# Kernel tuning notes

Measured on AMD Instinct MI355X. Metric: run time of the kernel, lower is better.

Reference implementation:

```python
import jax, jax.numpy as jnp
import numpy as np
import math

B, L, N, DIM, H = 2, 8, 1024, 512, 8
DH = DIM // H

def setup_inputs() -> dict:
    key = jax.random.key(0)
    ks = jax.random.split(key, 9)
    s = 1.0 / math.sqrt(DIM)
    return {
        "x": jax.random.normal(ks[0], (B, L, N, DIM), dtype=jnp.float32),
        "Wq": jax.random.normal(ks[1], (DIM, DIM), dtype=jnp.float32) * s,
        "bq": jnp.zeros((DIM,), dtype=jnp.float32),
        "Wk": jax.random.normal(ks[2], (DIM, DIM), dtype=jnp.float32) * s,
        "bk": jnp.zeros((DIM,), dtype=jnp.float32),
        "Wv": jax.random.normal(ks[3], (DIM, DIM), dtype=jnp.float32) * s,
        "bv": jnp.zeros((DIM,), dtype=jnp.float32),
        "Wo": jax.random.normal(ks[4], (DIM, DIM), dtype=jnp.float32) * s,
        "bo": jnp.zeros((DIM,), dtype=jnp.float32),
    }

def _split_heads(t):
    # 'b l n (h d) -> b l h n d'
    b, l, n, _ = t.shape
    return t.reshape(b, l, n, H, DH).transpose(0, 1, 3, 2, 4)

def reference(x, Wq, bq, Wk, bk, Wv, bv, Wo, bo):
    q = _split_heads(x @ Wq.T + bq)
    # FAITHFUL BUG: source maps (q, v, k) -> (q_mat, k_mat, v_mat),
    # so the "keys" come from the v projection and "values" from the k projection.
    k_mat = _split_heads(x @ Wv.T + bv)
    v_mat = _split_heads(x @ Wk.T + bk)
    # scale is sqrt(Dh * num_heads) = sqrt(dim), as in the source
    scores = jnp.einsum('blhnd,blhmd->blhnm', q, k_mat) / math.sqrt(DIM)
    weights = jax.nn.softmax(scores, axis=-1)
    inter = jnp.einsum('blhnm,blhmd->blhnd', weights, v_mat)
    # 'b l h n d -> b l n (h d)'
    inter = inter.transpose(0, 1, 3, 2, 4).reshape(x.shape[0], x.shape[1], x.shape[2], DIM)
    return inter @ Wo.T + bo
```

## Files before the change

### kernel.cpp

```cpp
#include <hip/hip_runtime.h>
#include <stdint.h>

#define DIMC 512
#define NSEQ 1024
#define BLT  16
#define NHEAD 8
#define DHD  64
#define MTOT (BLT*NSEQ)

typedef float f32x4 __attribute__((ext_vector_type(4)));
typedef float f32x16 __attribute__((ext_vector_type(16)));
typedef short s16x8 __attribute__((ext_vector_type(8)));
typedef short s16x4 __attribute__((ext_vector_type(4)));

__device__ __forceinline__ unsigned short f2bf(float f) {
    unsigned int u = __float_as_uint(f);
    u += 0x7fffu + ((u >> 16) & 1u);
    return (unsigned short)(u >> 16);
}
__device__ __forceinline__ float bf2f(unsigned short h) {
    return __uint_as_float(((unsigned int)h) << 16);
}

#define QSCALE (0.04419417382415922f * 1.4426950408889634f)

__device__ __forceinline__ void gll16(const void* g, void* l) {
    __builtin_amdgcn_global_load_lds(
        (const __attribute__((address_space(1))) void*)g,
        (__attribute__((address_space(3))) void*)l, 16, 0, 0);
}

__device__ __forceinline__ unsigned int cvtpk(float lo, float hi) {
    unsigned int r;
    asm("v_cvt_pk_bf16_f32 %0, %1, %2" : "=v"(r) : "v"(lo), "v"(hi));
    return r;
}

__device__ __forceinline__ void pl32swap(unsigned int &a, unsigned int &b) {
    asm volatile("v_permlane32_swap_b32 %0, %1" : "+v"(a), "+v"(b));
}

__device__ __forceinline__ bool detect_bf16(const unsigned short* x) {
    int t = threadIdx.x & 63;
    unsigned short v = x[2 * t];
    int e = (v >> 7) & 0xFF;
    unsigned long long ball = __ballot(e < 100 || e > 137);
    return __popcll(ball) < 16;
}

struct ConvArgs {
    const void* src[9];
    unsigned short* dst[9];
};

__global__ __launch_bounds__(256) void conv_kernel(ConvArgs a,
                                                   const unsigned short* __restrict__ xdet) {
    const bool isbf = detect_bf16(xdet);
    int b = blockIdx.x;
    int seg, idx;
    if (b < 4096)      { seg = 0; idx = (b * 256 + threadIdx.x) * 8; }
    else if (b < 4608) { int t = b - 4096; seg = 1 + (t >> 7);
                         idx = (((t & 127) * 256) + threadIdx.x) * 8; }
    else               { int i = threadIdx.x * 8; seg = 5 + (i >> 9); idx = i & 511; }
    const void* s = a.src[seg];
    unsigned short* d = a.dst[seg];
    if (isbf) {
        *(uint4*)(d + idx) = *(const uint4*)((const unsigned short*)s + idx);
    } else {
        float4 t0 = *(const float4*)((const float*)s + idx);
        float4 t1 = *(const float4*)((const float*)s + idx + 4);
        ushort4 v0{f2bf(t0.x), f2bf(t0.y), f2bf(t0.z), f2bf(t0.w)};
        ushort4 v1{f2bf(t1.x), f2bf(t1.y), f2bf(t1.z), f2bf(t1.w)};
        *(ushort4*)(d + idx)     = v0;
        *(ushort4*)(d + idx + 4) = v1;
    }
}

__device__ __forceinline__ void gemm_core_async(
    const unsigned short* __restrict__ Ap, const unsigned short* __restrict__ Wp,
    int mBase, int nBase, unsigned short* Al, unsigned short* Bl, f32x4 acc[4][4])
{
    const int wave = threadIdx.x >> 6;
    const int lane = threadIdx.x & 63;
    const int lr = lane & 15, lg = lane >> 4;
    const int wm = wave >> 1, wn = wave & 1;
    const int srow = lane >> 3;
    const int scol = (lane & 7) * 8;

    #pragma unroll
    for (int a = 0; a < 4; ++a)
        #pragma unroll
        for (int b = 0; b < 4; ++b) acc[a][b] = (f32x4){0.f, 0.f, 0.f, 0.f};

    for (int k0 = 0; k0 < DIMC; k0 += 64) {
        #pragma unroll
        for (int i = 0; i < 4; ++i) {
            int rbase = (wave * 4 + i) * 8;
            gll16(Ap + (long)(mBase + rbase + srow) * DIMC + k0 + scol, Al + rbase * 64);
            gll16(Wp + (long)(nBase + rbase + srow) * DIMC + k0 + scol, Bl + rbase * 64);
        }
        __syncthreads();

        #pragma unroll
        for (int kk = 0; kk < 64; kk += 32) {
            s16x8 af[4], bf_[4];
            #pragma unroll
            for (int a = 0; a < 4; ++a)
                af[a] = *(const s16x8*)&Al[(wm * 64 + a * 16 + lr) * 64 + kk + lg * 8];
            #pragma unroll
            for (int b = 0; b < 4; ++b)
                bf_[b] = *(const s16x8*)&Bl[(wn * 64 + b * 16 + lr) * 64 + kk + lg * 8];
            #pragma unroll
            for (int a = 0; a < 4; ++a)
                #pragma unroll
                for (int b = 0; b < 4; ++b)
                    acc[a][b] = __builtin_amdgcn_mfma_f32_16x16x32_bf16(af[a], bf_[b], acc[a][b], 0, 0, 0);
        }
        __syncthreads();
    }
}

__global__ __launch_bounds__(256) void proj_kernel(
    const unsigned short* __restrict__ xb,
    const unsigned short* __restrict__ Wqb, const unsigned short* __restrict__ Wkb,
    const unsigned short* __restrict__ Wvb,
    const unsigned short* __restrict__ bqb, const unsigned short* __restrict__ bkb,
    const unsigned short* __restrict__ bvb,
    unsigned short* __restrict__ Q, unsigned short* __restrict__ K,
    unsigned short* __restrict__ Vt)
{
    const int z = blockIdx.z;
    const unsigned short* Wp = (z == 0) ? Wqb : ((z == 1) ? Wvb : Wkb);
    const unsigned short* bp = (z == 0) ? bqb : ((z == 1) ? bvb : bkb);
    unsigned short* outp = (z == 0) ? Q : ((z == 1) ? K : Vt);
    const float oscale = (z == 0) ? QSCALE : 1.0f;

    const int mBase = blockIdx.x * 128;
    const int nBase = blockIdx.y * 128;
    const int lane = threadIdx.x & 63;
    const int lr = lane & 15, lg = lane >> 4;
    const int wm = (threadIdx.x >> 6) >> 1, wn = (threadIdx.x >> 6) & 1;

    __shared__ unsigned short Al[128 * 64];
    __shared__ unsigned short Bl[128 * 64];
    f32x4 acc[4][4];
    gemm_core_async(xb, Wp, mBase, nBase, Al, Bl, acc);

    #pragma unroll
    for (int b = 0; b < 4; ++b) {
        int j = nBase + wn * 64 + b * 16 + lr;
        float bb = bf2f(bp[j]);
        int h = j >> 6, d = j & 63;
        #pragma unroll
        for (int a = 0; a < 4; ++a) {
            int m0 = mBase + wm * 64 + a * 16 + lg * 4;
            int bl = m0 >> 10, n0 = m0 & 1023;
            if (z == 2) {
                ushort4 pk;
                unsigned short* p = (unsigned short*)&pk;
                #pragma unroll
                for (int r = 0; r < 4; ++r) p[r] = f2bf(acc[a][b][r] + bb);
                *(ushort4*)&outp[(((bl << 3) + h) << 16) + (d << 10) + n0] = pk;
            } else {
                #pragma unroll
                for (int r = 0; r < 4; ++r) {
                    float v = (acc[a][b][r] + bb) * oscale;
                    outp[(((bl << 3) + h) << 16) + ((n0 + r) << 6) + d] = f2bf(v);
                }
            }
        }
    }
}

__global__ __launch_bounds__(256) void out_gemm_kernel(
    const unsigned short* __restrict__ inter, const unsigned short* __restrict__ Wob,
    const unsigned short* __restrict__ bob, void* __restrict__ outp,
    const unsigned short* __restrict__ xdet)
{
    const bool isbf = detect_bf16(xdet);
    const int mBase = blockIdx.x * 128;
    const int nBase = blockIdx.y * 128;
    const int lane = threadIdx.x & 63;
    const int lr = lane & 15, lg = lane >> 4;
    const int wm = (threadIdx.x >> 6) >> 1, wn = (threadIdx.x >> 6) & 1;

    __shared__ unsigned short Al[128 * 64];
    __shared__ unsigned short Bl[128 * 64];
    f32x4 acc[4][4];
    gemm_core_async(inter, Wob, mBase, nBase, Al, Bl, acc);

    #pragma unroll
    for (int b = 0; b < 4; ++b) {
        int j = nBase + wn * 64 + b * 16 + lr;
        float bb = bf2f(bob[j]);
        #pragma unroll
        for (int a = 0; a < 4; ++a) {
            #pragma unroll
            for (int r = 0; r < 4; ++r) {
                long m = mBase + wm * 64 + a * 16 + lg * 4 + r;
                float v = acc[a][b][r] + bb;
                if (isbf) ((unsigned short*)outp)[m * DIMC + j] = f2bf(v);
                else      ((float*)outp)[m * DIMC + j] = v;
            }
        }
    }
}

#define SWZ(row, col) ((row) * 64 + ((col) ^ (((row) & 7) * 8)))

__global__ __launch_bounds__(256, 3) void attn_kernel(
    const unsigned short* __restrict__ Q, const unsigned short* __restrict__ K,
    const unsigned short* __restrict__ Vt, unsigned short* __restrict__ inter)
{
    const int b = blockIdx.x;
    const int bh = b & 127;
    const int qt = b >> 7;
    const int tid = threadIdx.x;
    const int wave = tid >> 6;
    const int lane = tid & 63;
    const int l31 = lane & 31;
    const int hi = lane >> 5;

    const unsigned short* Qb = Q + (long)bh * (NSEQ * DHD);
    const int qbase = qt * 128 + wave * 32;

    s16x8 qf[4];
    #pragma unroll
    for (int k16 = 0; k16 < 4; ++k16)
        qf[k16] = *(const s16x8*)&Qb[(qbase + l31) * DHD + k16 * 16 + hi * 8];

    __shared__ unsigned short Kl[2][64 * 64];
    __shared__ unsigned short Vl[2][64 * 64];

    const int srow = tid >> 3;
    const int scol = ((tid & 7) * 8) ^ ((srow & 7) * 8);
    const unsigned short* kp = K  + (long)bh * (NSEQ * DHD) + srow * DHD  + scol;
    const unsigned short* vp = Vt + (long)bh * (NSEQ * DHD) + srow * NSEQ + scol;

    auto stage = [&](int buf, long ko, long vo) {
        unsigned short* Kb_ = &Kl[buf][0];
        unsigned short* Vb_ = &Vl[buf][0];
        gll16(kp + ko,         Kb_ + wave * 512);
        gll16(kp + ko + 2048,  Kb_ + wave * 512 + 2048);
        gll16(vp + vo,         Vb_ + wave * 512);
        gll16(vp + vo + 32768, Vb_ + wave * 512 + 2048);
    };

    f32x16 o[2];
    f32x16 lacc;
    f32x16 zero16;
    #pragma unroll
    for (int r = 0; r < 16; ++r) { o[0][r] = 0.f; o[1][r] = 0.f; lacc[r] = 0.f; zero16[r] = 0.f; }
    const s16x8 ones8 = {(short)0x3F80, (short)0x3F80, (short)0x3F80, (short)0x3F80,
                         (short)0x3F80, (short)0x3F80, (short)0x3F80, (short)0x3F80};

    stage(0, 0, 0);
    __syncthreads();

    #pragma unroll 2
    for (int kt = 0; kt < 16; ++kt) {
        const int cur = kt & 1;
        if (kt < 15)
            stage(cur ^ 1, (long)(kt + 1) * (64 * DHD), (long)(kt + 1) * 64);

        const unsigned short* Kc = &Kl[cur][0];
        const unsigned short* Vc = &Vl[cur][0];

        #pragma unroll
        for (int kc = 0; kc < 2; ++kc) {
            s16x8 af[4];
            #pragma unroll
            for (int k16 = 0; k16 < 4; ++k16)
                af[k16] = *(const s16x8*)&Kc[SWZ(kc * 32 + l31, k16 * 16 + hi * 8)];
            f32x16 s;
            __builtin_amdgcn_s_setprio(1);
            s = __builtin_amdgcn_mfma_f32_32x32x16_bf16(af[0], qf[0], zero16, 0, 0, 0);
            s = __builtin_amdgcn_mfma_f32_32x32x16_bf16(af[1], qf[1], s, 0, 0, 0);
            s = __builtin_amdgcn_mfma_f32_32x32x16_bf16(af[2], qf[2], s, 0, 0, 0);
            s = __builtin_amdgcn_mfma_f32_32x32x16_bf16(af[3], qf[3], s, 0, 0, 0);
            __builtin_amdgcn_s_setprio(0);

            float p[16];
            #pragma unroll
            for (int r = 0; r < 16; ++r) p[r] = __builtin_exp2f(s[r]);
            unsigned int w[4][2];
            #pragma unroll
            for (int b4 = 0; b4 < 4; ++b4) {
                w[b4][0] = cvtpk(p[4 * b4 + 0], p[4 * b4 + 1]);
                w[b4][1] = cvtpk(p[4 * b4 + 2], p[4 * b4 + 3]);
            }
            s16x8 frag[2];
            #pragma unroll
            for (int t16 = 0; t16 < 2; ++t16) {
                unsigned int a0 = w[2 * t16][0], b0 = w[2 * t16 + 1][0];
                unsigned int a1 = w[2 * t16][1], b1 = w[2 * t16 + 1][1];
                pl32swap(a0, b0);
                pl32swap(a1, b1);
                union { unsigned int u[4]; s16x8 v; } f;
                f.u[0] = a0; f.u[1] = a1; f.u[2] = b0; f.u[3] = b1;
                frag[t16] = f.v;
            }

            s16x8 va[2][2];
            #pragma unroll
            for (int dt = 0; dt < 2; ++dt)
                #pragma unroll
                for (int t16 = 0; t16 < 2; ++t16)
                    va[dt][t16] = *(const s16x8*)&Vc[SWZ(dt * 32 + l31, kc * 32 + t16 * 16 + hi * 8)];
            __builtin_amdgcn_s_setprio(1);
            lacc = __builtin_amdgcn_mfma_f32_32x32x16_bf16(ones8, frag[0], lacc, 0, 0, 0);
            lacc = __builtin_amdgcn_mfma_f32_32x32x16_bf16(ones8, frag[1], lacc, 0, 0, 0);
            #pragma unroll
            for (int dt = 0; dt < 2; ++dt)
                #pragma unroll
                for (int t16 = 0; t16 < 2; ++t16)
                    o[dt] = __builtin_amdgcn_mfma_f32_32x32x16_bf16(va[dt][t16], frag[t16], o[dt], 0, 0, 0);
            __builtin_amdgcn_s_setprio(0);
        }

        if (kt < 15) __syncthreads();
    }

    const int bl = bh >> 3, h = bh & 7;
    const int q = qbase + l31;
    float inv = 1.f / lacc[0];
    #pragma unroll
    for (int dt = 0; dt < 2; ++dt) {
        #pragma unroll
        for (int b4 = 0; b4 < 4; ++b4) {
            unsigned int w0 = cvtpk(o[dt][4 * b4 + 0] * inv, o[dt][4 * b4 + 1] * inv);
            unsigned int w1 = cvtpk(o[dt][4 * b4 + 2] * inv, o[dt][4 * b4 + 3] * inv);
            union { unsigned int u[2]; ushort4 v; } pk;
            pk.u[0] = w0; pk.u[1] = w1;
            *(ushort4*)&inter[((long)(bl * NSEQ + q)) * DIMC + h * 64 + dt * 32 + 8 * b4 + 4 * hi] = pk.v;
        }
    }
}

extern "C" void kernel_launch(void* const* d_in, const int* in_sizes, int n_in,
                              void* d_out, int out_size, void* d_ws, size_t ws_size,
                              hipStream_t stream) {
    const void* x  = d_in[0];
    const void* Wq = d_in[1]; const void* bq = d_in[2];
    const void* Wk = d_in[3]; const void* bk = d_in[4];
    const void* Wv = d_in[5]; const void* bv = d_in[6];
    const void* Wo = d_in[7]; const void* bo = d_in[8];

    char* ws = (char*)d_ws;
    unsigned short* xb  = (unsigned short*)ws;
    unsigned short* Q   = xb + (long)MTOT * DIMC;
    unsigned short* K   = Q  + (long)MTOT * DIMC;
    unsigned short* Vt  = K  + (long)MTOT * DIMC;
    unsigned short* Wqb = Vt + (long)MTOT * DIMC;
    unsigned short* Wkb = Wqb + DIMC * DIMC;
    unsigned short* Wvb = Wkb + DIMC * DIMC;
    unsigned short* Wob = Wvb + DIMC * DIMC;
    unsigned short* bqb = Wob + DIMC * DIMC;
    unsigned short* bkb = bqb + DIMC;
    unsigned short* bvb = bkb + DIMC;
    unsigned short* bob = bvb + DIMC;

    ConvArgs ca;
    ca.src[0] = x;  ca.src[1] = Wq; ca.src[2] = Wk; ca.src[3] = Wv; ca.src[4] = Wo;
    ca.src[5] = bq; ca.src[6] = bk; ca.src[7] = bv; ca.src[8] = bo;
    ca.dst[0] = xb;  ca.dst[1] = Wqb; ca.dst[2] = Wkb; ca.dst[3] = Wvb; ca.dst[4] = Wob;
    ca.dst[5] = bqb; ca.dst[6] = bkb; ca.dst[7] = bvb; ca.dst[8] = bob;
    conv_kernel<<<4609, 256, 0, stream>>>(ca, (const unsigned short*)x);

    dim3 gp(MTOT / 128, DIMC / 128, 3);
    proj_kernel<<<gp, 256, 0, stream>>>(xb, Wqb, Wkb, Wvb, bqb, bkb, bvb, Q, K, Vt);

    attn_kernel<<<8 * 128, 256, 0, stream>>>(Q, K, Vt, xb );

    dim3 go(MTOT / 128, DIMC / 128);
    out_gemm_kernel<<<go, 256, 0, stream>>>(xb , Wob, bob, d_out,
                                            (const unsigned short*)x);
}
```

Baseline: 219.3 us.

## Pre-swizzle K and V tiles in projection output and halve attention block size

The projection kernel now writes K with an XOR swizzle already applied and V in a tiled layout that matches the MFMA fragment order, so the attention kernel can load contiguous 2048-element chunks straight into LDS with no per-thread address swizzle. The attention kernel shrinks to 128 threads (2 waves, 64 queries per block) with 32-key tiles, launching twice as many blocks. This is meant to simplify LDS staging, reduce LDS use per block and raise occupancy. In exchange there are twice as many loop iterations and barriers per block, and each block does less work to amortize its fixed costs.

```diff
diff --git a/kernel.cpp b/kernel.cpp
--- a/kernel.cpp
+++ b/kernel.cpp
@@ -160,7 +160,16 @@
                 unsigned short* p = (unsigned short*)&pk;
                 #pragma unroll
                 for (int r = 0; r < 4; ++r) p[r] = f2bf(acc[a][b][r] + bb);
-                *(ushort4*)&outp[(((bl << 3) + h) << 16) + (d << 10) + n0] = pk;
+                int base = (((bl << 3) + h) << 16) + ((n0 >> 5) << 11)
+                         + (((n0 >> 3) & 3) << 9) + (d << 3) + (n0 & 7);
+                *(ushort4*)&outp[base] = pk;
+            } else if (z == 1) {
+                #pragma unroll
+                for (int r = 0; r < 4; ++r) {
+                    int n = n0 + r;
+                    float v = acc[a][b][r] + bb;
+                    outp[(((bl << 3) + h) << 16) + (n << 6) + (d ^ ((n & 7) << 3))] = f2bf(v);
+                }
             } else {
                 #pragma unroll
                 for (int r = 0; r < 4; ++r) {
@@ -206,9 +215,7 @@
     }
 }
 
-#define SWZ(row, col) ((row) * 64 + ((col) ^ (((row) & 7) * 8)))
-
-__global__ __launch_bounds__(256, 3) void attn_kernel(
+__global__ __launch_bounds__(128, 4) void attn_kernel(
     const unsigned short* __restrict__ Q, const unsigned short* __restrict__ K,
     const unsigned short* __restrict__ Vt, unsigned short* __restrict__ inter)
 {
@@ -222,28 +229,27 @@
     const int hi = lane >> 5;
 
     const unsigned short* Qb = Q + (long)bh * (NSEQ * DHD);
-    const int qbase = qt * 128 + wave * 32;
+    const int qbase = qt * 64 + wave * 32;
 
     s16x8 qf[4];
     #pragma unroll
     for (int k16 = 0; k16 < 4; ++k16)
         qf[k16] = *(const s16x8*)&Qb[(qbase + l31) * DHD + k16 * 16 + hi * 8];
 
-    __shared__ unsigned short Kl[2][64 * 64];
-    __shared__ unsigned short Vl[2][64 * 64];
-
-    const int srow = tid >> 3;
-    const int scol = ((tid & 7) * 8) ^ ((srow & 7) * 8);
-    const unsigned short* kp = K  + (long)bh * (NSEQ * DHD) + srow * DHD  + scol;
-    const unsigned short* vp = Vt + (long)bh * (NSEQ * DHD) + srow * NSEQ + scol;
-
-    auto stage = [&](int buf, long ko, long vo) {
+    __shared__ unsigned short Kl[2][32 * 64];
+    __shared__ unsigned short Vl[2][32 * 64];
+
+    const unsigned short* kg = K  + (long)bh * (NSEQ * DHD);
+    const unsigned short* vg = Vt + (long)bh * (NSEQ * DHD);
+
+    auto stage = [&](int buf, int kt) {
         unsigned short* Kb_ = &Kl[buf][0];
         unsigned short* Vb_ = &Vl[buf][0];
-        gll16(kp + ko,         Kb_ + wave * 512);
-        gll16(kp + ko + 2048,  Kb_ + wave * 512 + 2048);
-        gll16(vp + vo,         Vb_ + wave * 512);
-        gll16(vp + vo + 32768, Vb_ + wave * 512 + 2048);
+        const int u8 = tid * 8;
+        gll16(kg + kt * 2048 + u8,        Kb_ + wave * 512);
+        gll16(kg + kt * 2048 + u8 + 1024, Kb_ + wave * 512 + 1024);
+        gll16(vg + kt * 2048 + u8,        Vb_ + wave * 512);
+        gll16(vg + kt * 2048 + u8 + 1024, Vb_ + wave * 512 + 1024);
     };
 
     f32x16 o[2];
@@ -254,71 +260,69 @@
     const s16x8 ones8 = {(short)0x3F80, (short)0x3F80, (short)0x3F80, (short)0x3F80,
                          (short)0x3F80, (short)0x3F80, (short)0x3F80, (short)0x3F80};
 
-    stage(0, 0, 0);
+    stage(0, 0);
     __syncthreads();
 
     #pragma unroll 2
-    for (int kt = 0; kt < 16; ++kt) {
+    for (int kt = 0; kt < 32; ++kt) {
         const int cur = kt & 1;
-        if (kt < 15)
-            stage(cur ^ 1, (long)(kt + 1) * (64 * DHD), (long)(kt + 1) * 64);
+        if (kt < 31)
+            stage(cur ^ 1, kt + 1);
 
         const unsigned short* Kc = &Kl[cur][0];
         const unsigned short* Vc = &Vl[cur][0];
 
-        #pragma unroll
-        for (int kc = 0; kc < 2; ++kc) {
-            s16x8 af[4];
-            #pragma unroll
-            for (int k16 = 0; k16 < 4; ++k16)
-                af[k16] = *(const s16x8*)&Kc[SWZ(kc * 32 + l31, k16 * 16 + hi * 8)];
-            f32x16 s;
-            __builtin_amdgcn_s_setprio(1);
-            s = __builtin_amdgcn_mfma_f32_32x32x16_bf16(af[0], qf[0], zero16, 0, 0, 0);
-            s = __builtin_amdgcn_mfma_f32_32x32x16_bf16(af[1], qf[1], s, 0, 0, 0);
-            s = __builtin_amdgcn_mfma_f32_32x32x16_bf16(af[2], qf[2], s, 0, 0, 0);
-            s = __builtin_amdgcn_mfma_f32_32x32x16_bf16(af[3], qf[3], s, 0, 0, 0);
-            __builtin_amdgcn_s_setprio(0);
-
-            float p[16];
-            #pragma unroll
-            for (int r = 0; r < 16; ++r) p[r] = __builtin_exp2f(s[r]);
-            unsigned int w[4][2];
-            #pragma unroll
-            for (int b4 = 0; b4 < 4; ++b4) {
-                w[b4][0] = cvtpk(p[4 * b4 + 0], p[4 * b4 + 1]);
-                w[b4][1] = cvtpk(p[4 * b4 + 2], p[4 * b4 + 3]);
-            }
-            s16x8 frag[2];
-            #pragma unroll
-            for (int t16 = 0; t16 < 2; ++t16) {
-                unsigned int a0 = w[2 * t16][0], b0 = w[2 * t16 + 1][0];
-                unsigned int a1 = w[2 * t16][1], b1 = w[2 * t16 + 1][1];
-                pl32swap(a0, b0);
-                pl32swap(a1, b1);
-                union { unsigned int u[4]; s16x8 v; } f;
-                f.u[0] = a0; f.u[1] = a1; f.u[2] = b0; f.u[3] = b1;
-                frag[t16] = f.v;
-            }
-
-            s16x8 va[2][2];
-            #pragma unroll
-            for (int dt = 0; dt < 2; ++dt)
-                #pragma unroll
-                for (int t16 = 0; t16 < 2; ++t16)
-                    va[dt][t16] = *(const s16x8*)&Vc[SWZ(dt * 32 + l31, kc * 32 + t16 * 16 + hi * 8)];
-            __builtin_amdgcn_s_setprio(1);
-            lacc = __builtin_amdgcn_mfma_f32_32x32x16_bf16(ones8, frag[0], lacc, 0, 0, 0);
-            lacc = __builtin_amdgcn_mfma_f32_32x32x16_bf16(ones8, frag[1], lacc, 0, 0, 0);
-            #pragma unroll
-            for (int dt = 0; dt < 2; ++dt)
-                #pragma unroll
-                for (int t16 = 0; t16 < 2; ++t16)
-                    o[dt] = __builtin_amdgcn_mfma_f32_32x32x16_bf16(va[dt][t16], frag[t16], o[dt], 0, 0, 0);
-            __builtin_amdgcn_s_setprio(0);
-        }
-
-        if (kt < 15) __syncthreads();
+        s16x8 af[4];
+        #pragma unroll
+        for (int k16 = 0; k16 < 4; ++k16)
+            af[k16] = *(const s16x8*)&Kc[l31 * 64 + ((k16 * 16 + hi * 8) ^ ((l31 & 7) * 8))];
+        f32x16 s;
+        __builtin_amdgcn_s_setprio(1);
+        s = __builtin_amdgcn_mfma_f32_32x32x16_bf16(af[0], qf[0], zero16, 0, 0, 0);
+        s = __builtin_amdgcn_mfma_f32_32x32x16_bf16(af[1], qf[1], s, 0, 0, 0);
+        s = __builtin_amdgcn_mfma_f32_32x32x16_bf16(af[2], qf[2], s, 0, 0, 0);
+        s = __builtin_amdgcn_mfma_f32_32x32x16_bf16(af[3], qf[3], s, 0, 0, 0);
+        __builtin_amdgcn_s_setprio(0);
+
+        float p[16];
+        #pragma unroll
+        for (int r = 0; r < 16; ++r) p[r] = __builtin_exp2f(s[r]);
+        unsigned int w[4][2];
+        #pragma unroll
+        for (int b4 = 0; b4 < 4; ++b4) {
+            w[b4][0] = cvtpk(p[4 * b4 + 0], p[4 * b4 + 1]);
+            w[b4][1] = cvtpk(p[4 * b4 + 2], p[4 * b4 + 3]);
+        }
+        s16x8 frag[2];
+        #pragma unroll
+        for (int t16 = 0; t16 < 2; ++t16) {
+            unsigned int a0 = w[2 * t16][0], b0 = w[2 * t16 + 1][0];
+            unsigned int a1 = w[2 * t16][1], b1 = w[2 * t16 + 1][1];
+            pl32swap(a0, b0);
+            pl32swap(a1, b1);
+            union { unsigned int u[4]; s16x8 v; } f;
+            f.u[0] = a0; f.u[1] = a1; f.u[2] = b0; f.u[3] = b1;
+            frag[t16] = f.v;
+        }
+
+        s16x8 va[2][2];
+        #pragma unroll
+        for (int dt = 0; dt < 2; ++dt)
+            #pragma unroll
+            for (int t16 = 0; t16 < 2; ++t16)
+                va[dt][t16] = *(const s16x8*)&Vc[((t16 * 2 + hi) * 64 + dt * 32 + l31) * 8];
+
+        __builtin_amdgcn_s_setprio(1);
+        lacc = __builtin_amdgcn_mfma_f32_32x32x16_bf16(ones8, frag[0], lacc, 0, 0, 0);
+        lacc = __builtin_amdgcn_mfma_f32_32x32x16_bf16(ones8, frag[1], lacc, 0, 0, 0);
+        #pragma unroll
+        for (int dt = 0; dt < 2; ++dt)
+            #pragma unroll
+            for (int t16 = 0; t16 < 2; ++t16)
+                o[dt] = __builtin_amdgcn_mfma_f32_32x32x16_bf16(va[dt][t16], frag[t16], o[dt], 0, 0, 0);
+        __builtin_amdgcn_s_setprio(0);
+
+        if (kt < 31) __syncthreads();
     }
 
     const int bl = bh >> 3, h = bh & 7;
@@ -370,7 +374,7 @@
     dim3 gp(MTOT / 128, DIMC / 128, 3);
     proj_kernel<<<gp, 256, 0, stream>>>(xb, Wqb, Wkb, Wvb, bqb, bkb, bvb, Q, K, Vt);
 
-    attn_kernel<<<8 * 128, 256, 0, stream>>>(Q, K, Vt, xb );
+    attn_kernel<<<16 * 128, 128, 0, stream>>>(Q, K, Vt, xb );
 
     dim3 go(MTOT / 128, DIMC / 128);
     out_gemm_kernel<<<go, 256, 0, stream>>>(xb , Wob, bob, d_out,
```

After: 222.9 us. No clear change (+1.6%).
